# Performance work log

Hardware: AMD Instinct MI355X
Metric: run time of the kernel (lower is better)

## Reference

```python
import jax, jax.numpy as jnp
import numpy as np

B, H, S, D = 8, 8, 2048, 64
NEG = -1e9


def setup_inputs() -> dict:
    key = jax.random.key(0)
    k1, k2, k3, k4 = jax.random.split(key, 4)
    query = jax.random.normal(k1, (B, H, S, D), dtype=jnp.float32)
    kk = jax.random.normal(k2, (B, H, S, D), dtype=jnp.float32)
    value = jax.random.normal(k3, (B, H, S, D), dtype=jnp.float32)
    mask = jax.random.randint(k4, (B, S, S), 0, 2, dtype=jnp.int32)
    return {"query": query, "key": kk, "value": value, "mask": mask}


def reference(query, key, value, mask):
    dk = key.shape[-1]
    # scores: [B,H,S,S] = (q/sqrt(dk)) @ k^T
    scores = jnp.einsum('bhqd,bhkd->bhqk', query / np.sqrt(dk), key)
    # mask broadcast over heads: [B,1,S,S]
    scores = jnp.where(mask[:, None, :, :] == 0, NEG, scores)
    attn = jax.nn.softmax(scores.astype(jnp.float32), axis=-1).astype(query.dtype)
    # dropout is identity in eval/deterministic reference
    return jnp.einsum('bhqk,bhkd->bhqd', attn, value)
```

## Files before the change

kernel.cpp:

```cpp
#include <hip/hip_runtime.h>
#include <hip/hip_bf16.h>
#include <stdint.h>


#define B_ 8
#define H_ 8
#define S_ 2048
#define D_ 64
#define QT 128
#define KT 64
#define NT (S_ / KT)
#define TILE_E (KT * D_)
#define LOG2E 1.44269504088896340736f
#define QSCALE (0.125f * LOG2E)

typedef __bf16 bf16;
typedef bf16 bf16x8 __attribute__((ext_vector_type(8)));
typedef float f32x4 __attribute__((ext_vector_type(4)));
typedef unsigned short ushort8_t __attribute__((ext_vector_type(8)));
typedef unsigned long long u64;

#if __has_builtin(__builtin_amdgcn_exp2f)
#define EXP2(x) __builtin_amdgcn_exp2f(x)
#else
#define EXP2(x) exp2f(x)
#endif

static __device__ __forceinline__ unsigned short bfb(float f) {
    bf16 h = (bf16)f;
    return __builtin_bit_cast(unsigned short, h);
}
static __device__ __forceinline__ int phi_inv(int c) {
    return ((c >> 5) & 1) * 32 + ((c >> 2) & 1) * 16 + ((c >> 4) & 1) * 8 +
           ((c >> 3) & 1) * 4 + (c & 3);
}
static __device__ __forceinline__ void gload16(const unsigned short* g, unsigned short* l) {
    __builtin_amdgcn_global_load_lds(
        (const __attribute__((address_space(1))) unsigned int*)g,
        (__attribute__((address_space(3))) unsigned int*)l, 16, 0, 0);
}

#define KV_BLOCKS (B_ * H_ * NT)

__global__ __launch_bounds__(256) void prep_fused(
    const float* __restrict__ K, const float* __restrict__ V,
    unsigned short* __restrict__ Ko, unsigned short* __restrict__ Vo,
    const int* __restrict__ M, u64* __restrict__ W) {
    const int tid = threadIdx.x;
    if (blockIdx.x >= KV_BLOCKS) {
        const int ln = tid & 63;
        const int w0 = (blockIdx.x - KV_BLOCKS) * 32 + (tid >> 6) * 8;
#pragma unroll
        for (int j = 0; j < 8; ++j) {
            const int v = M[(long)(w0 + j) * 64 + ln];
            const u64 bal = __ballot(v != 0);
            if (ln == 0) W[w0 + j] = bal;
        }
        return;
    }
    if (Ko == nullptr) return;
    __shared__ float Vl[64][65];
    const int t = blockIdx.x & (NT - 1);
    const int bh = blockIdx.x >> 5;
    const float* Kg = K + ((long)bh * S_ + t * 64) * D_;
    const float* Vg = V + ((long)bh * S_ + t * 64) * D_;
    unsigned short* Kout = Ko + ((long)bh * S_ + t * 64) * D_;
    unsigned short* Vout = Vo + (long)bh * D_ * S_ + t * 64;
    {
        const int kv = tid >> 2, d0 = (tid & 3) * 16;
#pragma unroll
        for (int half = 0; half < 2; ++half) {
            const float4 f0 = *(const float4*)(Kg + kv * D_ + d0 + half * 8);
            const float4 f1 = *(const float4*)(Kg + kv * D_ + d0 + half * 8 + 4);
            ushort8_t u;
            u[0] = bfb(f0.x); u[1] = bfb(f0.y); u[2] = bfb(f0.z); u[3] = bfb(f0.w);
            u[4] = bfb(f1.x); u[5] = bfb(f1.y); u[6] = bfb(f1.z); u[7] = bfb(f1.w);
            *(ushort8_t*)(Kout + kv * D_ + d0 + half * 8) = u;
        }
    }
    {
#pragma unroll
        for (int i = 0; i < 4; ++i) {
            const int kv = i * 16 + (tid >> 4);
            const int d4 = (tid & 15) * 4;
            const float4 f = *(const float4*)(Vg + kv * D_ + d4);
            Vl[kv][d4 + 0] = f.x; Vl[kv][d4 + 1] = f.y;
            Vl[kv][d4 + 2] = f.z; Vl[kv][d4 + 3] = f.w;
        }
    }
    __syncthreads();
    {
#pragma unroll
        for (int j = 0; j < 4; ++j) {
            const int chunk = j * 256 + tid;
            const int d = chunk >> 4, q4 = chunk & 15;
            ushort4 w;
            w.x = bfb(Vl[phi_inv(q4 * 4 + 0)][d]);
            w.y = bfb(Vl[phi_inv(q4 * 4 + 1)][d]);
            w.z = bfb(Vl[phi_inv(q4 * 4 + 2)][d]);
            w.w = bfb(Vl[phi_inv(q4 * 4 + 3)][d]);
            *(ushort4*)(Vout + (long)d * S_ + q4 * 4) = w;
        }
    }
}

template <int MODE>
__global__ __launch_bounds__(512, 4) void attn_fwd(
    const float* __restrict__ Q, const float* __restrict__ K,
    const float* __restrict__ V, const int* __restrict__ M,
    const u64* __restrict__ W, const unsigned short* __restrict__ Kp,
    const unsigned short* __restrict__ Vp, float* __restrict__ O)
{
    __shared__ __attribute__((aligned(16))) unsigned short Ks3[4 * TILE_E];
    __shared__ __attribute__((aligned(16))) unsigned short Vt3[4 * TILE_E];

    const int tid = threadIdx.x;
    const int wv = tid >> 6, ln = tid & 63;
    const int col = ln & 15, grp = ln >> 4;

    int bid = blockIdx.x;
    bid = (bid & 7) * 128 + (bid >> 3);
    const int qt = bid & 15;
    const int h = (bid >> 4) & 7;
    const int b = bid >> 7;
    const int qw = qt * QT + wv * 16;

    const float* Qg = Q + ((long)((b * H_ + h) * S_) + qw + col) * D_;
    bf16x8 qf[2];
#pragma unroll
    for (int c = 0; c < 2; ++c) {
        const float4 a0 = *(const float4*)(Qg + c * 32 + grp * 8);
        const float4 a1 = *(const float4*)(Qg + c * 32 + grp * 8 + 4);
        qf[c][0] = (bf16)(a0.x * QSCALE); qf[c][1] = (bf16)(a0.y * QSCALE);
        qf[c][2] = (bf16)(a0.z * QSCALE); qf[c][3] = (bf16)(a0.w * QSCALE);
        qf[c][4] = (bf16)(a1.x * QSCALE); qf[c][5] = (bf16)(a1.y * QSCALE);
        qf[c][6] = (bf16)(a1.z * QSCALE); qf[c][7] = (bf16)(a1.w * QSCALE);
    }
    bf16x8 onesf;
#pragma unroll
    for (int j = 0; j < 8; ++j) onesf[j] = (bf16)1.0f;

    f32x4 oacc[4];
#pragma unroll
    for (int i = 0; i < 4; ++i) oacc[i] = (f32x4){0.f, 0.f, 0.f, 0.f};
    f32x4 accs = (f32x4){0.f, 0.f, 0.f, 0.f};

    const u64* Wg = (MODE >= 1) ? (W + ((long)b * S_ + qw + col) * (S_ / 64)) : nullptr;
    const int* Mg = (MODE == 0) ? (M + ((long)b * S_ + qw + col) * S_) : nullptr;
    const unsigned short* Kbh = Kp + (long)(b * H_ + h) * S_ * D_;
    const unsigned short* Vbh = Vp + (long)(b * H_ + h) * D_ * S_;
    const float* Kf = K + (long)(b * H_ + h) * S_ * D_;
    const float* Vf = V + (long)(b * H_ + h) * S_ * D_;

    const int rl = ln >> 3;
    const int c8 = (ln & 7) ^ rl;
    const int krow = wv * 8 + rl;

    float4 ka[2];
    float va[8];
    const int vd = ln, kg0 = wv;

    auto STAGE_ISSUE = [&](int kv0, int buf) {
        gload16(Kbh + (long)(kv0 + krow) * D_ + c8 * 8, Ks3 + buf * TILE_E + wv * 512);
        gload16(Vbh + (long)krow * S_ + kv0 + c8 * 8, Vt3 + buf * TILE_E + wv * 512);
    };
    auto LOADT = [&](int kv0) {
#pragma unroll
        for (int i = 0; i < 2; ++i) {
            const int idx4 = i * 512 + tid;
            const int row = idx4 >> 4, c4 = idx4 & 15;
            ka[i] = *(const float4*)(Kf + (long)(kv0 + row) * D_ + c4 * 4);
        }
#pragma unroll
        for (int i = 0; i < 2; ++i) {
            const int kg = kg0 + i * 8;
            const int kvn = phi_inv(kg * 4);
#pragma unroll
            for (int j = 0; j < 4; ++j)
                va[i * 4 + j] = Vf[(long)(kv0 + kvn + j) * D_ + vd];
        }
    };
    auto WRITET = [&](int buf) {
#pragma unroll
        for (int i = 0; i < 2; ++i) {
            const int idx4 = i * 512 + tid;
            const int row = idx4 >> 4, c4 = idx4 & 15;
            const int byte = (row * 128 + c4 * 8) ^ ((row & 7) << 4);
            ushort4 w;
            w.x = bfb(ka[i].x); w.y = bfb(ka[i].y);
            w.z = bfb(ka[i].z); w.w = bfb(ka[i].w);
            *(ushort4*)((char*)(Ks3 + buf * TILE_E) + byte) = w;
        }
#pragma unroll
        for (int i = 0; i < 2; ++i) {
            const int kg = kg0 + i * 8;
            const int byte = (vd * 128 + kg * 8) ^ ((vd & 7) << 4);
            ushort4 w;
            w.x = bfb(va[i * 4 + 0]); w.y = bfb(va[i * 4 + 1]);
            w.z = bfb(va[i * 4 + 2]); w.w = bfb(va[i * 4 + 3]);
            *(ushort4*)((char*)(Vt3 + buf * TILE_E) + byte) = w;
        }
    };

    auto QKB = [&](u64 mwfull, const unsigned short* Kc, f32x4* sc) {
        const u64 mws = mwfull >> (grp * 4);
        const unsigned mlo = (unsigned)mws, mhi = (unsigned)(mws >> 32);
#pragma unroll
        for (int blk = 0; blk < 4; ++blk) {
            const unsigned w32 = (blk < 2) ? mlo : mhi;
#pragma unroll
            for (int r = 0; r < 4; ++r) {
                const int bit = (blk & 1) * 16 + r;
                sc[blk][r] = ((w32 >> bit) & 1u) ? 0.0f : -1e9f;
            }
        }
        __builtin_amdgcn_s_setprio(1);
#pragma unroll
        for (int blk = 0; blk < 4; ++blk) {
            const int row = blk * 16 + col;
            const int byte0 = (row * 128 + grp * 16) ^ ((row & 7) << 4);
            const int byte1 = (row * 128 + 64 + grp * 16) ^ ((row & 7) << 4);
            const bf16x8 kf0 = *(const bf16x8*)((const char*)Kc + byte0);
            const bf16x8 kf1 = *(const bf16x8*)((const char*)Kc + byte1);
            sc[blk] = __builtin_amdgcn_mfma_f32_16x16x32_bf16(kf0, qf[0], sc[blk], 0, 0, 0);
            sc[blk] = __builtin_amdgcn_mfma_f32_16x16x32_bf16(kf1, qf[1], sc[blk], 0, 0, 0);
        }
        __builtin_amdgcn_s_setprio(0);
    };
    auto SMPV = [&](f32x4* sc, const unsigned short* Vc) {
        bf16x8 pf[2];
#pragma unroll
        for (int c = 0; c < 2; ++c)
#pragma unroll
            for (int j = 0; j < 8; ++j)
                pf[c][j] = (bf16)EXP2(sc[2 * c + (j >> 2)][j & 3]);
        __builtin_amdgcn_s_setprio(1);
        accs = __builtin_amdgcn_mfma_f32_16x16x32_bf16(pf[0], onesf, accs, 0, 0, 0);
        accs = __builtin_amdgcn_mfma_f32_16x16x32_bf16(pf[1], onesf, accs, 0, 0, 0);
#pragma unroll
        for (int c = 0; c < 2; ++c)
#pragma unroll
            for (int db = 0; db < 4; ++db) {
                const int vrow = db * 16 + col;
                const int byte = (vrow * 128 + c * 64 + grp * 16) ^ ((vrow & 7) << 4);
                const bf16x8 vf = *(const bf16x8*)((const char*)Vc + byte);
                oacc[db] = __builtin_amdgcn_mfma_f32_16x16x32_bf16(pf[c], vf, oacc[db], 0, 0, 0);
            }
        __builtin_amdgcn_s_setprio(0);
    };

#define WAIT2_BAR() do { asm volatile("s_waitcnt vmcnt(2)" ::: "memory"); \
    __builtin_amdgcn_s_barrier(); __builtin_amdgcn_sched_barrier(0); } while (0)
#define WAIT0_BAR() do { asm volatile("s_waitcnt vmcnt(0)" ::: "memory"); \
    __builtin_amdgcn_s_barrier(); __builtin_amdgcn_sched_barrier(0); } while (0)

    if (MODE == 2) {
        f32x4 scA[4], scB[4];
        STAGE_ISSUE(0, 0);
        STAGE_ISSUE(KT, 1);
        WAIT2_BAR();
        {
            const u64 mw0 = Wg[0];
            QKB(mw0, Ks3, scA);
            STAGE_ISSUE(2 * KT, 2);
        }
        WAIT2_BAR();
#pragma unroll 1
        for (int tt = 0; tt < NT - 4; tt += 4) {
#pragma unroll
            for (int j = 0; j < 4; ++j) {
                const int t = tt + j;
                const u64 mwn = Wg[t + 1];
                STAGE_ISSUE((t + 3) * KT, (j + 3) & 3);
                if ((j & 1) == 0) {
                    QKB(mwn, Ks3 + ((j + 1) & 3) * TILE_E, scB);
                    SMPV(scA, Vt3 + j * TILE_E);
                } else {
                    QKB(mwn, Ks3 + ((j + 1) & 3) * TILE_E, scA);
                    SMPV(scB, Vt3 + j * TILE_E);
                }
                WAIT2_BAR();
            }
        }
        {
            const u64 mw29 = Wg[NT - 3];
            STAGE_ISSUE((NT - 1) * KT, (NT - 1) & 3);
            QKB(mw29, Ks3 + ((NT - 3) & 3) * TILE_E, scB);
            SMPV(scA, Vt3 + ((NT - 4) & 3) * TILE_E);
            WAIT2_BAR();
            const u64 mw30 = Wg[NT - 2];
            QKB(mw30, Ks3 + ((NT - 2) & 3) * TILE_E, scA);
            SMPV(scB, Vt3 + ((NT - 3) & 3) * TILE_E);
            WAIT0_BAR();
            const u64 mw31 = Wg[NT - 1];
            QKB(mw31, Ks3 + ((NT - 1) & 3) * TILE_E, scB);
            SMPV(scA, Vt3 + ((NT - 2) & 3) * TILE_E);
            SMPV(scB, Vt3 + ((NT - 1) & 3) * TILE_E);
        }
    } else {
        auto FSTEP = [&](u64 mwfull, int t, const unsigned short* Kc, const unsigned short* Vc) {
            f32x4 sc[4];
            const f32x4 zq = (f32x4){0.f, 0.f, 0.f, 0.f};
#pragma unroll
            for (int blk = 0; blk < 4; ++blk) {
                const int row = blk * 16 + col;
                const int byte0 = (row * 128 + grp * 16) ^ ((row & 7) << 4);
                const int byte1 = (row * 128 + 64 + grp * 16) ^ ((row & 7) << 4);
                const bf16x8 kf0 = *(const bf16x8*)((const char*)Kc + byte0);
                const bf16x8 kf1 = *(const bf16x8*)((const char*)Kc + byte1);
                sc[blk] = __builtin_amdgcn_mfma_f32_16x16x32_bf16(kf0, qf[0], zq, 0, 0, 0);
                sc[blk] = __builtin_amdgcn_mfma_f32_16x16x32_bf16(kf1, qf[1], sc[blk], 0, 0, 0);
            }
            bf16x8 pf[2];
            if (MODE >= 1) {
                const u64 mws = mwfull >> (grp * 4);
                const unsigned mlo = (unsigned)mws, mhi = (unsigned)(mws >> 32);
#pragma unroll
                for (int c = 0; c < 2; ++c)
#pragma unroll
                    for (int j = 0; j < 8; ++j) {
                        const int blk = 2 * c + (j >> 2), r = j & 3;
                        const unsigned w32 = (blk < 2) ? mlo : mhi;
                        const int bit = (blk & 1) * 16 + r;
                        const float s = ((w32 >> bit) & 1u) ? sc[blk][r] : -1e9f;
                        pf[c][j] = (bf16)EXP2(s);
                    }
            } else {
#pragma unroll
                for (int c = 0; c < 2; ++c)
#pragma unroll
                    for (int j = 0; j < 8; ++j) {
                        const int blk = 2 * c + (j >> 2), r = j & 3;
                        const int mv = Mg[t * KT + blk * 16 + grp * 4 + r];
                        const float s = mv ? sc[blk][r] : -1e9f;
                        pf[c][j] = (bf16)EXP2(s);
                    }
            }
            accs = __builtin_amdgcn_mfma_f32_16x16x32_bf16(pf[0], onesf, accs, 0, 0, 0);
            accs = __builtin_amdgcn_mfma_f32_16x16x32_bf16(pf[1], onesf, accs, 0, 0, 0);
#pragma unroll
            for (int c = 0; c < 2; ++c)
#pragma unroll
                for (int db = 0; db < 4; ++db) {
                    const int vrow = db * 16 + col;
                    const int byte = (vrow * 128 + c * 64 + grp * 16) ^ ((vrow & 7) << 4);
                    const bf16x8 vf = *(const bf16x8*)((const char*)Vc + byte);
                    oacc[db] = __builtin_amdgcn_mfma_f32_16x16x32_bf16(pf[c], vf, oacc[db], 0, 0, 0);
                }
        };
        LOADT(0);
        WRITET(0);
        __syncthreads();
#pragma unroll 1
        for (int t = 0; t < NT; t += 2) {
            if (t + 1 < NT) LOADT((t + 1) * KT);
            FSTEP(MODE >= 1 ? Wg[t] : 0ull, t, Ks3, Vt3);
            if (t + 1 < NT) WRITET(1);
            __syncthreads();
            if (t + 2 < NT) LOADT((t + 2) * KT);
            FSTEP(MODE >= 1 ? Wg[t + 1] : 0ull, t + 1, Ks3 + TILE_E, Vt3 + TILE_E);
            if (t + 2 < NT) WRITET(0);
            __syncthreads();
        }
    }

    float* Og = O + ((long)((b * H_ + h) * S_) + qw) * D_;
#pragma unroll
    for (int r = 0; r < 4; ++r) {
        const float inv = 1.0f / accs[r];
#pragma unroll
        for (int db = 0; db < 4; ++db)
            Og[(grp * 4 + r) * D_ + db * 16 + col] = oacc[db][r] * inv;
    }
#undef WAIT2_BAR
#undef WAIT0_BAR
}

extern "C" void kernel_launch(void* const* d_in, const int* in_sizes, int n_in,
                              void* d_out, int out_size, void* d_ws, size_t ws_size,
                              hipStream_t stream) {
    (void)in_sizes; (void)n_in; (void)out_size;
    const float* Q = (const float*)d_in[0];
    const float* K = (const float*)d_in[1];
    const float* V = (const float*)d_in[2];
    const int*   M = (const int*)d_in[3];
    float* O = (float*)d_out;

    const size_t szW = (size_t)B_ * S_ * (S_ / 64) * sizeof(u64);
    const size_t szK = (size_t)B_ * H_ * S_ * D_ * 2;
    const int grid = B_ * H_ * (S_ / QT);
    const int nmaskblk = (B_ * S_ * (S_ / 64)) / 32;

    if (ws_size >= szW + 2 * szK) {
        u64* W = (u64*)d_ws;
        unsigned short* Kp = (unsigned short*)((char*)d_ws + szW);
        unsigned short* Vp = (unsigned short*)((char*)d_ws + szW + szK);
        prep_fused<<<KV_BLOCKS + nmaskblk, 256, 0, stream>>>(K, V, Kp, Vp, M, W);
        attn_fwd<2><<<grid, 512, 0, stream>>>(Q, K, V, M, W, Kp, Vp, O);
    } else if (ws_size >= szW) {
        u64* W = (u64*)d_ws;
        prep_fused<<<KV_BLOCKS + nmaskblk, 256, 0, stream>>>(K, V, nullptr, nullptr, M, W);
        attn_fwd<1><<<grid, 512, 0, stream>>>(Q, K, V, M, W, nullptr, nullptr, O);
    } else {
        attn_fwd<0><<<grid, 512, 0, stream>>>(Q, K, V, M, nullptr, nullptr, nullptr, O);
    }
}
```

Measured before the change: 157.0 us.

## Split main attention path into 256-thread kernel with two query tiles per wave

The workspace path now uses a new attn_main kernel with 4 waves per block, where each wave handles 32 query rows (two 16-row tiles). Each K and V fragment read from LDS feeds MFMAs for both tiles, which halves LDS reads per unit of work. The old software pipeline that overlapped the next tile's QK with the current softmax·V is replaced by a simpler prefetch-2 loop that computes QK and PV in the same step. This raises register pressure and gives up that cross-stage overlap, with the intent of getting more MFMA work per LDS load and per barrier.

```diff
diff --git a/kernel.cpp b/kernel.cpp
--- a/kernel.cpp
+++ b/kernel.cpp
@@ -104,15 +104,203 @@
     }
 }
 
-template <int MODE>
-__global__ __launch_bounds__(512, 4) void attn_fwd(
-    const float* __restrict__ Q, const float* __restrict__ K,
-    const float* __restrict__ V, const int* __restrict__ M,
-    const u64* __restrict__ W, const unsigned short* __restrict__ Kp,
-    const unsigned short* __restrict__ Vp, float* __restrict__ O)
+__global__ __launch_bounds__(256, 2) void attn_main(
+    const float* __restrict__ Q, const u64* __restrict__ W,
+    const unsigned short* __restrict__ Kp, const unsigned short* __restrict__ Vp,
+    float* __restrict__ O)
 {
     __shared__ __attribute__((aligned(16))) unsigned short Ks3[4 * TILE_E];
     __shared__ __attribute__((aligned(16))) unsigned short Vt3[4 * TILE_E];
+
+    const int tid = threadIdx.x;
+    const int wv = tid >> 6, ln = tid & 63;
+    const int col = ln & 15, grp = ln >> 4;
+
+    int bid = blockIdx.x;
+    bid = (bid & 7) * 128 + (bid >> 3);
+    const int qt = bid & 15;
+    const int h = (bid >> 4) & 7;
+    const int b = bid >> 7;
+    const int qa = qt * QT + wv * 32;
+
+    bf16x8 qfa[2], qfb[2];
+    {
+        const float* Qga = Q + ((long)((b * H_ + h) * S_) + qa + col) * D_;
+        const float* Qgb = Qga + 16 * D_;
+#pragma unroll
+        for (int c = 0; c < 2; ++c) {
+            const float4 a0 = *(const float4*)(Qga + c * 32 + grp * 8);
+            const float4 a1 = *(const float4*)(Qga + c * 32 + grp * 8 + 4);
+            qfa[c][0] = (bf16)(a0.x * QSCALE); qfa[c][1] = (bf16)(a0.y * QSCALE);
+            qfa[c][2] = (bf16)(a0.z * QSCALE); qfa[c][3] = (bf16)(a0.w * QSCALE);
+            qfa[c][4] = (bf16)(a1.x * QSCALE); qfa[c][5] = (bf16)(a1.y * QSCALE);
+            qfa[c][6] = (bf16)(a1.z * QSCALE); qfa[c][7] = (bf16)(a1.w * QSCALE);
+            const float4 b0 = *(const float4*)(Qgb + c * 32 + grp * 8);
+            const float4 b1 = *(const float4*)(Qgb + c * 32 + grp * 8 + 4);
+            qfb[c][0] = (bf16)(b0.x * QSCALE); qfb[c][1] = (bf16)(b0.y * QSCALE);
+            qfb[c][2] = (bf16)(b0.z * QSCALE); qfb[c][3] = (bf16)(b0.w * QSCALE);
+            qfb[c][4] = (bf16)(b1.x * QSCALE); qfb[c][5] = (bf16)(b1.y * QSCALE);
+            qfb[c][6] = (bf16)(b1.z * QSCALE); qfb[c][7] = (bf16)(b1.w * QSCALE);
+        }
+    }
+    bf16x8 onesf;
+#pragma unroll
+    for (int j = 0; j < 8; ++j) onesf[j] = (bf16)1.0f;
+
+    f32x4 oaccA[4], oaccB[4];
+#pragma unroll
+    for (int i = 0; i < 4; ++i) {
+        oaccA[i] = (f32x4){0.f, 0.f, 0.f, 0.f};
+        oaccB[i] = (f32x4){0.f, 0.f, 0.f, 0.f};
+    }
+    f32x4 accsA = (f32x4){0.f, 0.f, 0.f, 0.f};
+    f32x4 accsB = (f32x4){0.f, 0.f, 0.f, 0.f};
+
+    const u64* Wa = W + ((long)b * S_ + qa + col) * (S_ / 64);
+    const u64* Wb = Wa + 16 * (S_ / 64);
+    const unsigned short* Kbh = Kp + (long)(b * H_ + h) * S_ * D_;
+    const unsigned short* Vbh = Vp + (long)(b * H_ + h) * D_ * S_;
+
+    const int rl = ln >> 3;
+    const int c8 = (ln & 7) ^ rl;
+
+    auto STAGE_ISSUE = [&](int kv0, int buf) {
+#pragma unroll
+        for (int i = 0; i < 2; ++i) {
+            const int row = i * 32 + wv * 8 + rl;
+            gload16(Kbh + (long)(kv0 + row) * D_ + c8 * 8,
+                    Ks3 + buf * TILE_E + i * 2048 + wv * 512);
+            gload16(Vbh + (long)row * S_ + kv0 + c8 * 8,
+                    Vt3 + buf * TILE_E + i * 2048 + wv * 512);
+        }
+    };
+
+    auto STEP = [&](u64 mwa, u64 mwb, const unsigned short* Kc, const unsigned short* Vc) {
+        f32x4 sa[4], sb[4];
+        {
+            const u64 ma = mwa >> (grp * 4), mb = mwb >> (grp * 4);
+            const unsigned alo = (unsigned)ma, ahi = (unsigned)(ma >> 32);
+            const unsigned blo = (unsigned)mb, bhi = (unsigned)(mb >> 32);
+#pragma unroll
+            for (int blk = 0; blk < 4; ++blk) {
+                const unsigned wa32 = (blk < 2) ? alo : ahi;
+                const unsigned wb32 = (blk < 2) ? blo : bhi;
+#pragma unroll
+                for (int r = 0; r < 4; ++r) {
+                    const int bit = (blk & 1) * 16 + r;
+                    sa[blk][r] = ((wa32 >> bit) & 1u) ? 0.0f : -1e9f;
+                    sb[blk][r] = ((wb32 >> bit) & 1u) ? 0.0f : -1e9f;
+                }
+            }
+        }
+        __builtin_amdgcn_s_setprio(1);
+#pragma unroll
+        for (int blk = 0; blk < 4; ++blk) {
+            const int row = blk * 16 + col;
+            const int byte0 = (row * 128 + grp * 16) ^ ((row & 7) << 4);
+            const int byte1 = (row * 128 + 64 + grp * 16) ^ ((row & 7) << 4);
+            const bf16x8 kf0 = *(const bf16x8*)((const char*)Kc + byte0);
+            const bf16x8 kf1 = *(const bf16x8*)((const char*)Kc + byte1);
+            sa[blk] = __builtin_amdgcn_mfma_f32_16x16x32_bf16(kf0, qfa[0], sa[blk], 0, 0, 0);
+            sa[blk] = __builtin_amdgcn_mfma_f32_16x16x32_bf16(kf1, qfa[1], sa[blk], 0, 0, 0);
+            sb[blk] = __builtin_amdgcn_mfma_f32_16x16x32_bf16(kf0, qfb[0], sb[blk], 0, 0, 0);
+            sb[blk] = __builtin_amdgcn_mfma_f32_16x16x32_bf16(kf1, qfb[1], sb[blk], 0, 0, 0);
+        }
+        __builtin_amdgcn_s_setprio(0);
+        bf16x8 pa[2], pb[2];
+#pragma unroll
+        for (int c = 0; c < 2; ++c)
+#pragma unroll
+            for (int j = 0; j < 8; ++j) {
+                const int blk = 2 * c + (j >> 2), r = j & 3;
+                pa[c][j] = (bf16)EXP2(sa[blk][r]);
+                pb[c][j] = (bf16)EXP2(sb[blk][r]);
+            }
+        __builtin_amdgcn_s_setprio(1);
+        accsA = __builtin_amdgcn_mfma_f32_16x16x32_bf16(pa[0], onesf, accsA, 0, 0, 0);
+        accsA = __builtin_amdgcn_mfma_f32_16x16x32_bf16(pa[1], onesf, accsA, 0, 0, 0);
+        accsB = __builtin_amdgcn_mfma_f32_16x16x32_bf16(pb[0], onesf, accsB, 0, 0, 0);
+        accsB = __builtin_amdgcn_mfma_f32_16x16x32_bf16(pb[1], onesf, accsB, 0, 0, 0);
+#pragma unroll
+        for (int c = 0; c < 2; ++c)
+#pragma unroll
+            for (int db = 0; db < 4; ++db) {
+                const int vrow = db * 16 + col;
+                const int byte = (vrow * 128 + c * 64 + grp * 16) ^ ((vrow & 7) << 4);
+                const bf16x8 vf = *(const bf16x8*)((const char*)Vc + byte);
+                oaccA[db] = __builtin_amdgcn_mfma_f32_16x16x32_bf16(pa[c], vf, oaccA[db], 0, 0, 0);
+                oaccB[db] = __builtin_amdgcn_mfma_f32_16x16x32_bf16(pb[c], vf, oaccB[db], 0, 0, 0);
+            }
+        __builtin_amdgcn_s_setprio(0);
+    };
+
+#define WAIT4_BAR() do { asm volatile("s_waitcnt vmcnt(4)" ::: "memory"); \
+    __builtin_amdgcn_s_barrier(); __builtin_amdgcn_sched_barrier(0); } while (0)
+#define WAIT0_BAR() do { asm volatile("s_waitcnt vmcnt(0)" ::: "memory"); \
+    __builtin_amdgcn_s_barrier(); __builtin_amdgcn_sched_barrier(0); } while (0)
+
+    STAGE_ISSUE(0, 0);
+    STAGE_ISSUE(KT, 1);
+    WAIT4_BAR();
+
+#pragma unroll 1
+    for (int tt = 0; tt < NT - 4; tt += 4) {
+#pragma unroll
+        for (int j = 0; j < 4; ++j) {
+            const int t = tt + j;
+            const u64 mwa = Wa[t], mwb = Wb[t];
+            STAGE_ISSUE((t + 2) * KT, (j + 2) & 3);
+            STEP(mwa, mwb, Ks3 + j * TILE_E, Vt3 + j * TILE_E);
+            WAIT4_BAR();
+        }
+    }
+    {
+        {
+            const u64 mwa = Wa[NT - 4], mwb = Wb[NT - 4];
+            STAGE_ISSUE((NT - 2) * KT, (NT - 2) & 3);
+            STEP(mwa, mwb, Ks3 + ((NT - 4) & 3) * TILE_E, Vt3 + ((NT - 4) & 3) * TILE_E);
+            WAIT4_BAR();
+        }
+        {
+            const u64 mwa = Wa[NT - 3], mwb = Wb[NT - 3];
+            STAGE_ISSUE((NT - 1) * KT, (NT - 1) & 3);
+            STEP(mwa, mwb, Ks3 + ((NT - 3) & 3) * TILE_E, Vt3 + ((NT - 3) & 3) * TILE_E);
+            WAIT4_BAR();
+        }
+        {
+            const u64 mwa = Wa[NT - 2], mwb = Wb[NT - 2];
+            STEP(mwa, mwb, Ks3 + ((NT - 2) & 3) * TILE_E, Vt3 + ((NT - 2) & 3) * TILE_E);
+            WAIT0_BAR();
+        }
+        {
+            const u64 mwa = Wa[NT - 1], mwb = Wb[NT - 1];
+            STEP(mwa, mwb, Ks3 + ((NT - 1) & 3) * TILE_E, Vt3 + ((NT - 1) & 3) * TILE_E);
+        }
+    }
+
+    float* Oa = O + ((long)((b * H_ + h) * S_) + qa) * D_;
+#pragma unroll
+    for (int r = 0; r < 4; ++r) {
+        const float ia = 1.0f / accsA[r];
+        const float ib = 1.0f / accsB[r];
+#pragma unroll
+        for (int db = 0; db < 4; ++db) {
+            Oa[(grp * 4 + r) * D_ + db * 16 + col] = oaccA[db][r] * ia;
+            Oa[(16 + grp * 4 + r) * D_ + db * 16 + col] = oaccB[db][r] * ib;
+        }
+    }
+#undef WAIT4_BAR
+#undef WAIT0_BAR
+}
+
+template <int MODE>
+__global__ __launch_bounds__(512, 4) void attn_fb(
+    const float* __restrict__ Q, const float* __restrict__ K,
+    const float* __restrict__ V, const int* __restrict__ M,
+    const u64* __restrict__ W, float* __restrict__ O)
+{
+    __shared__ __attribute__((aligned(16))) unsigned short Ks2[2 * TILE_E];
+    __shared__ __attribute__((aligned(16))) unsigned short Vt2[2 * TILE_E];
 
     const int tid = threadIdx.x;
     const int wv = tid >> 6, ln = tid & 63;
@@ -147,23 +335,13 @@
 
     const u64* Wg = (MODE >= 1) ? (W + ((long)b * S_ + qw + col) * (S_ / 64)) : nullptr;
     const int* Mg = (MODE == 0) ? (M + ((long)b * S_ + qw + col) * S_) : nullptr;
-    const unsigned short* Kbh = Kp + (long)(b * H_ + h) * S_ * D_;
-    const unsigned short* Vbh = Vp + (long)(b * H_ + h) * D_ * S_;
     const float* Kf = K + (long)(b * H_ + h) * S_ * D_;
     const float* Vf = V + (long)(b * H_ + h) * S_ * D_;
-
-    const int rl = ln >> 3;
-    const int c8 = (ln & 7) ^ rl;
-    const int krow = wv * 8 + rl;
 
     float4 ka[2];
     float va[8];
     const int vd = ln, kg0 = wv;
 
-    auto STAGE_ISSUE = [&](int kv0, int buf) {
-        gload16(Kbh + (long)(kv0 + krow) * D_ + c8 * 8, Ks3 + buf * TILE_E + wv * 512);
-        gload16(Vbh + (long)krow * S_ + kv0 + c8 * 8, Vt3 + buf * TILE_E + wv * 512);
-    };
     auto LOADT = [&](int kv0) {
 #pragma unroll
         for (int i = 0; i < 2; ++i) {
@@ -189,7 +367,7 @@
             ushort4 w;
             w.x = bfb(ka[i].x); w.y = bfb(ka[i].y);
             w.z = bfb(ka[i].z); w.w = bfb(ka[i].w);
-            *(ushort4*)((char*)(Ks3 + buf * TILE_E) + byte) = w;
+            *(ushort4*)((char*)(Ks2 + buf * TILE_E) + byte) = w;
         }
 #pragma unroll
         for (int i = 0; i < 2; ++i) {
@@ -198,23 +376,12 @@
             ushort4 w;
             w.x = bfb(va[i * 4 + 0]); w.y = bfb(va[i * 4 + 1]);
             w.z = bfb(va[i * 4 + 2]); w.w = bfb(va[i * 4 + 3]);
-            *(ushort4*)((char*)(Vt3 + buf * TILE_E) + byte) = w;
+            *(ushort4*)((char*)(Vt2 + buf * TILE_E) + byte) = w;
         }
     };
-
-    auto QKB = [&](u64 mwfull, const unsigned short* Kc, f32x4* sc) {
-        const u64 mws = mwfull >> (grp * 4);
-        const unsigned mlo = (unsigned)mws, mhi = (unsigned)(mws >> 32);
-#pragma unroll
-        for (int blk = 0; blk < 4; ++blk) {
-            const unsigned w32 = (blk < 2) ? mlo : mhi;
-#pragma unroll
-            for (int r = 0; r < 4; ++r) {
-                const int bit = (blk & 1) * 16 + r;
-                sc[blk][r] = ((w32 >> bit) & 1u) ? 0.0f : -1e9f;
-            }
-        }
-        __builtin_amdgcn_s_setprio(1);
+    auto FSTEP = [&](u64 mwfull, int t, const unsigned short* Kc, const unsigned short* Vc) {
+        f32x4 sc[4];
+        const f32x4 zq = (f32x4){0.f, 0.f, 0.f, 0.f};
 #pragma unroll
         for (int blk = 0; blk < 4; ++blk) {
             const int row = blk * 16 + col;
@@ -222,19 +389,34 @@
             const int byte1 = (row * 128 + 64 + grp * 16) ^ ((row & 7) << 4);
             const bf16x8 kf0 = *(const bf16x8*)((const char*)Kc + byte0);
             const bf16x8 kf1 = *(const bf16x8*)((const char*)Kc + byte1);
-            sc[blk] = __builtin_amdgcn_mfma_f32_16x16x32_bf16(kf0, qf[0], sc[blk], 0, 0, 0);
+            sc[blk] = __builtin_amdgcn_mfma_f32_16x16x32_bf16(kf0, qf[0], zq, 0, 0, 0);
             sc[blk] = __builtin_amdgcn_mfma_f32_16x16x32_bf16(kf1, qf[1], sc[blk], 0, 0, 0);
         }
-        __builtin_amdgcn_s_setprio(0);
-    };
-    auto SMPV = [&](f32x4* sc, const unsigned short* Vc) {
         bf16x8 pf[2];
-#pragma unroll
-        for (int c = 0; c < 2; ++c)
-#pragma unroll
-            for (int j = 0; j < 8; ++j)
-                pf[c][j] = (bf16)EXP2(sc[2 * c + (j >> 2)][j & 3]);
-        __builtin_amdgcn_s_setprio(1);
+        if (MODE >= 1) {
+            const u64 mws = mwfull >> (grp * 4);
+            const unsigned mlo = (unsigned)mws, mhi = (unsigned)(mws >> 32);
+#pragma unroll
+            for (int c = 0; c < 2; ++c)
+#pragma unroll
+                for (int j = 0; j < 8; ++j) {
+                    const int blk = 2 * c + (j >> 2), r = j & 3;
+                    const unsigned w32 = (blk < 2) ? mlo : mhi;
+                    const int bit = (blk & 1) * 16 + r;
+                    const float s = ((w32 >> bit) & 1u) ? sc[blk][r] : -1e9f;
+                    pf[c][j] = (bf16)EXP2(s);
+                }
+        } else {
+#pragma unroll
+            for (int c = 0; c < 2; ++c)
+#pragma unroll
+                for (int j = 0; j < 8; ++j) {
+                    const int blk = 2 * c + (j >> 2), r = j & 3;
+                    const int mv = Mg[t * KT + blk * 16 + grp * 4 + r];
+                    const float s = mv ? sc[blk][r] : -1e9f;
+                    pf[c][j] = (bf16)EXP2(s);
+                }
+        }
         accs = __builtin_amdgcn_mfma_f32_16x16x32_bf16(pf[0], onesf, accs, 0, 0, 0);
         accs = __builtin_amdgcn_mfma_f32_16x16x32_bf16(pf[1], onesf, accs, 0, 0, 0);
 #pragma unroll
@@ -246,122 +428,21 @@
                 const bf16x8 vf = *(const bf16x8*)((const char*)Vc + byte);
                 oacc[db] = __builtin_amdgcn_mfma_f32_16x16x32_bf16(pf[c], vf, oacc[db], 0, 0, 0);
             }
-        __builtin_amdgcn_s_setprio(0);
     };
 
-#define WAIT2_BAR() do { asm volatile("s_waitcnt vmcnt(2)" ::: "memory"); \
-    __builtin_amdgcn_s_barrier(); __builtin_amdgcn_sched_barrier(0); } while (0)
-#define WAIT0_BAR() do { asm volatile("s_waitcnt vmcnt(0)" ::: "memory"); \
-    __builtin_amdgcn_s_barrier(); __builtin_amdgcn_sched_barrier(0); } while (0)
-
-    if (MODE == 2) {
-        f32x4 scA[4], scB[4];
-        STAGE_ISSUE(0, 0);
-        STAGE_ISSUE(KT, 1);
-        WAIT2_BAR();
-        {
-            const u64 mw0 = Wg[0];
-            QKB(mw0, Ks3, scA);
-            STAGE_ISSUE(2 * KT, 2);
-        }
-        WAIT2_BAR();
+    LOADT(0);
+    WRITET(0);
+    __syncthreads();
 #pragma unroll 1
-        for (int tt = 0; tt < NT - 4; tt += 4) {
-#pragma unroll
-            for (int j = 0; j < 4; ++j) {
-                const int t = tt + j;
-                const u64 mwn = Wg[t + 1];
-                STAGE_ISSUE((t + 3) * KT, (j + 3) & 3);
-                if ((j & 1) == 0) {
-                    QKB(mwn, Ks3 + ((j + 1) & 3) * TILE_E, scB);
-                    SMPV(scA, Vt3 + j * TILE_E);
-                } else {
-                    QKB(mwn, Ks3 + ((j + 1) & 3) * TILE_E, scA);
-                    SMPV(scB, Vt3 + j * TILE_E);
-                }
-                WAIT2_BAR();
-            }
-        }
-        {
-            const u64 mw29 = Wg[NT - 3];
-            STAGE_ISSUE((NT - 1) * KT, (NT - 1) & 3);
-            QKB(mw29, Ks3 + ((NT - 3) & 3) * TILE_E, scB);
-            SMPV(scA, Vt3 + ((NT - 4) & 3) * TILE_E);
-            WAIT2_BAR();
-            const u64 mw30 = Wg[NT - 2];
-            QKB(mw30, Ks3 + ((NT - 2) & 3) * TILE_E, scA);
-            SMPV(scB, Vt3 + ((NT - 3) & 3) * TILE_E);
-            WAIT0_BAR();
-            const u64 mw31 = Wg[NT - 1];
-            QKB(mw31, Ks3 + ((NT - 1) & 3) * TILE_E, scB);
-            SMPV(scA, Vt3 + ((NT - 2) & 3) * TILE_E);
-            SMPV(scB, Vt3 + ((NT - 1) & 3) * TILE_E);
-        }
-    } else {
-        auto FSTEP = [&](u64 mwfull, int t, const unsigned short* Kc, const unsigned short* Vc) {
-            f32x4 sc[4];
-            const f32x4 zq = (f32x4){0.f, 0.f, 0.f, 0.f};
-#pragma unroll
-            for (int blk = 0; blk < 4; ++blk) {
-                const int row = blk * 16 + col;
-                const int byte0 = (row * 128 + grp * 16) ^ ((row & 7) << 4);
-                const int byte1 = (row * 128 + 64 + grp * 16) ^ ((row & 7) << 4);
-                const bf16x8 kf0 = *(const bf16x8*)((const char*)Kc + byte0);
-                const bf16x8 kf1 = *(const bf16x8*)((const char*)Kc + byte1);
-                sc[blk] = __builtin_amdgcn_mfma_f32_16x16x32_bf16(kf0, qf[0], zq, 0, 0, 0);
-                sc[blk] = __builtin_amdgcn_mfma_f32_16x16x32_bf16(kf1, qf[1], sc[blk], 0, 0, 0);
-            }
-            bf16x8 pf[2];
-            if (MODE >= 1) {
-                const u64 mws = mwfull >> (grp * 4);
-                const unsigned mlo = (unsigned)mws, mhi = (unsigned)(mws >> 32);
-#pragma unroll
-                for (int c = 0; c < 2; ++c)
-#pragma unroll
-                    for (int j = 0; j < 8; ++j) {
-                        const int blk = 2 * c + (j >> 2), r = j & 3;
-                        const unsigned w32 = (blk < 2) ? mlo : mhi;
-                        const int bit = (blk & 1) * 16 + r;
-                        const float s = ((w32 >> bit) & 1u) ? sc[blk][r] : -1e9f;
-                        pf[c][j] = (bf16)EXP2(s);
-                    }
-            } else {
-#pragma unroll
-                for (int c = 0; c < 2; ++c)
-#pragma unroll
-                    for (int j = 0; j < 8; ++j) {
-                        const int blk = 2 * c + (j >> 2), r = j & 3;
-                        const int mv = Mg[t * KT + blk * 16 + grp * 4 + r];
-                        const float s = mv ? sc[blk][r] : -1e9f;
-                        pf[c][j] = (bf16)EXP2(s);
-                    }
-            }
-            accs = __builtin_amdgcn_mfma_f32_16x16x32_bf16(pf[0], onesf, accs, 0, 0, 0);
-            accs = __builtin_amdgcn_mfma_f32_16x16x32_bf16(pf[1], onesf, accs, 0, 0, 0);
-#pragma unroll
-            for (int c = 0; c < 2; ++c)
-#pragma unroll
-                for (int db = 0; db < 4; ++db) {
-                    const int vrow = db * 16 + col;
-                    const int byte = (vrow * 128 + c * 64 + grp * 16) ^ ((vrow & 7) << 4);
-                    const bf16x8 vf = *(const bf16x8*)((const char*)Vc + byte);
-                    oacc[db] = __builtin_amdgcn_mfma_f32_16x16x32_bf16(pf[c], vf, oacc[db], 0, 0, 0);
-                }
-        };
-        LOADT(0);
-        WRITET(0);
+    for (int t = 0; t < NT; t += 2) {
+        if (t + 1 < NT) LOADT((t + 1) * KT);
+        FSTEP(MODE >= 1 ? Wg[t] : 0ull, t, Ks2, Vt2);
+        if (t + 1 < NT) WRITET(1);
         __syncthreads();
-#pragma unroll 1
-        for (int t = 0; t < NT; t += 2) {
-            if (t + 1 < NT) LOADT((t + 1) * KT);
-            FSTEP(MODE >= 1 ? Wg[t] : 0ull, t, Ks3, Vt3);
-            if (t + 1 < NT) WRITET(1);
-            __syncthreads();
-            if (t + 2 < NT) LOADT((t + 2) * KT);
-            FSTEP(MODE >= 1 ? Wg[t + 1] : 0ull, t + 1, Ks3 + TILE_E, Vt3 + TILE_E);
-            if (t + 2 < NT) WRITET(0);
-            __syncthreads();
-        }
+        if (t + 2 < NT) LOADT((t + 2) * KT);
+        FSTEP(MODE >= 1 ? Wg[t + 1] : 0ull, t + 1, Ks2 + TILE_E, Vt2 + TILE_E);
+        if (t + 2 < NT) WRITET(0);
+        __syncthreads();
     }
 
     float* Og = O + ((long)((b * H_ + h) * S_) + qw) * D_;
@@ -372,8 +453,6 @@
         for (int db = 0; db < 4; ++db)
             Og[(grp * 4 + r) * D_ + db * 16 + col] = oacc[db][r] * inv;
     }
-#undef WAIT2_BAR
-#undef WAIT0_BAR
 }
 
 extern "C" void kernel_launch(void* const* d_in, const int* in_sizes, int n_in,
@@ -396,12 +475,12 @@
         unsigned short* Kp = (unsigned short*)((char*)d_ws + szW);
         unsigned short* Vp = (unsigned short*)((char*)d_ws + szW + szK);
         prep_fused<<<KV_BLOCKS + nmaskblk, 256, 0, stream>>>(K, V, Kp, Vp, M, W);
-        attn_fwd<2><<<grid, 512, 0, stream>>>(Q, K, V, M, W, Kp, Vp, O);
+        attn_main<<<grid, 256, 0, stream>>>(Q, W, Kp, Vp, O);
     } else if (ws_size >= szW) {
         u64* W = (u64*)d_ws;
         prep_fused<<<KV_BLOCKS + nmaskblk, 256, 0, stream>>>(K, V, nullptr, nullptr, M, W);
-        attn_fwd<1><<<grid, 512, 0, stream>>>(Q, K, V, M, W, nullptr, nullptr, O);
+        attn_fb<1><<<grid, 512, 0, stream>>>(Q, K, V, M, W, O);
     } else {
-        attn_fwd<0><<<grid, 512, 0, stream>>>(Q, K, V, M, nullptr, nullptr, nullptr, O);
-    }
-}
+        attn_fb<0><<<grid, 512, 0, stream>>>(Q, K, V, M, nullptr, O);
+    }
+}
```

Result: slower. 164.8 us (+5.0%).

## Replace 4-stage software-pipelined attention loop with simple double buffer at higher occupancy

Applied to the files above, without the earlier changes.

The main path drops the 4-buffer, 2-ahead pipeline in which QK of the next tile overlapped softmax/PV of the current one. It now uses a plain 2-buffer loop with one async stage in flight and a full vmcnt(0) barrier each step. LDS is halved and launch bounds go from 4 to 8 blocks per SM, so occupancy is meant to hide latency instead of explicit pipelining. The risk is exposed load latency and more barrier stalls per tile. The fallback modes are split into a separate kernel and are otherwise unchanged.

```diff
diff --git a/kernel.cpp b/kernel.cpp
--- a/kernel.cpp
+++ b/kernel.cpp
@@ -104,15 +104,13 @@
     }
 }
 
-template <int MODE>
-__global__ __launch_bounds__(512, 4) void attn_fwd(
-    const float* __restrict__ Q, const float* __restrict__ K,
-    const float* __restrict__ V, const int* __restrict__ M,
-    const u64* __restrict__ W, const unsigned short* __restrict__ Kp,
-    const unsigned short* __restrict__ Vp, float* __restrict__ O)
+__global__ __launch_bounds__(512, 8) void attn_main(
+    const float* __restrict__ Q, const u64* __restrict__ W,
+    const unsigned short* __restrict__ Kp, const unsigned short* __restrict__ Vp,
+    float* __restrict__ O)
 {
-    __shared__ __attribute__((aligned(16))) unsigned short Ks3[4 * TILE_E];
-    __shared__ __attribute__((aligned(16))) unsigned short Vt3[4 * TILE_E];
+    __shared__ __attribute__((aligned(16))) unsigned short Ks2[2 * TILE_E];
+    __shared__ __attribute__((aligned(16))) unsigned short Vt2[2 * TILE_E];
 
     const int tid = threadIdx.x;
     const int wv = tid >> 6, ln = tid & 63;
@@ -145,73 +143,32 @@
     for (int i = 0; i < 4; ++i) oacc[i] = (f32x4){0.f, 0.f, 0.f, 0.f};
     f32x4 accs = (f32x4){0.f, 0.f, 0.f, 0.f};
 
-    const u64* Wg = (MODE >= 1) ? (W + ((long)b * S_ + qw + col) * (S_ / 64)) : nullptr;
-    const int* Mg = (MODE == 0) ? (M + ((long)b * S_ + qw + col) * S_) : nullptr;
+    const u64* Wg = W + ((long)b * S_ + qw + col) * (S_ / 64);
     const unsigned short* Kbh = Kp + (long)(b * H_ + h) * S_ * D_;
     const unsigned short* Vbh = Vp + (long)(b * H_ + h) * D_ * S_;
-    const float* Kf = K + (long)(b * H_ + h) * S_ * D_;
-    const float* Vf = V + (long)(b * H_ + h) * S_ * D_;
-
-    const int rl = ln >> 3;
-    const int c8 = (ln & 7) ^ rl;
-    const int krow = wv * 8 + rl;
-
-    float4 ka[2];
-    float va[8];
-    const int vd = ln, kg0 = wv;
+
+    const int srow = tid >> 3;
+    const int rl = srow & 7;
+    const int c8 = (tid & 7) ^ rl;
 
     auto STAGE_ISSUE = [&](int kv0, int buf) {
-        gload16(Kbh + (long)(kv0 + krow) * D_ + c8 * 8, Ks3 + buf * TILE_E + wv * 512);
-        gload16(Vbh + (long)krow * S_ + kv0 + c8 * 8, Vt3 + buf * TILE_E + wv * 512);
+        gload16(Kbh + (long)(kv0 + srow) * D_ + c8 * 8, Ks2 + buf * TILE_E + tid * 8);
+        gload16(Vbh + (long)srow * S_ + kv0 + c8 * 8, Vt2 + buf * TILE_E + tid * 8);
     };
-    auto LOADT = [&](int kv0) {
-#pragma unroll
-        for (int i = 0; i < 2; ++i) {
-            const int idx4 = i * 512 + tid;
-            const int row = idx4 >> 4, c4 = idx4 & 15;
-            ka[i] = *(const float4*)(Kf + (long)(kv0 + row) * D_ + c4 * 4);
-        }
-#pragma unroll
-        for (int i = 0; i < 2; ++i) {
-            const int kg = kg0 + i * 8;
-            const int kvn = phi_inv(kg * 4);
-#pragma unroll
-            for (int j = 0; j < 4; ++j)
-                va[i * 4 + j] = Vf[(long)(kv0 + kvn + j) * D_ + vd];
-        }
-    };
-    auto WRITET = [&](int buf) {
-#pragma unroll
-        for (int i = 0; i < 2; ++i) {
-            const int idx4 = i * 512 + tid;
-            const int row = idx4 >> 4, c4 = idx4 & 15;
-            const int byte = (row * 128 + c4 * 8) ^ ((row & 7) << 4);
-            ushort4 w;
-            w.x = bfb(ka[i].x); w.y = bfb(ka[i].y);
-            w.z = bfb(ka[i].z); w.w = bfb(ka[i].w);
-            *(ushort4*)((char*)(Ks3 + buf * TILE_E) + byte) = w;
-        }
-#pragma unroll
-        for (int i = 0; i < 2; ++i) {
-            const int kg = kg0 + i * 8;
-            const int byte = (vd * 128 + kg * 8) ^ ((vd & 7) << 4);
-            ushort4 w;
-            w.x = bfb(va[i * 4 + 0]); w.y = bfb(va[i * 4 + 1]);
-            w.z = bfb(va[i * 4 + 2]); w.w = bfb(va[i * 4 + 3]);
-            *(ushort4*)((char*)(Vt3 + buf * TILE_E) + byte) = w;
-        }
-    };
-
-    auto QKB = [&](u64 mwfull, const unsigned short* Kc, f32x4* sc) {
-        const u64 mws = mwfull >> (grp * 4);
-        const unsigned mlo = (unsigned)mws, mhi = (unsigned)(mws >> 32);
-#pragma unroll
-        for (int blk = 0; blk < 4; ++blk) {
-            const unsigned w32 = (blk < 2) ? mlo : mhi;
-#pragma unroll
-            for (int r = 0; r < 4; ++r) {
-                const int bit = (blk & 1) * 16 + r;
-                sc[blk][r] = ((w32 >> bit) & 1u) ? 0.0f : -1e9f;
+
+    auto STEP = [&](u64 mwfull, const unsigned short* Kc, const unsigned short* Vc) {
+        f32x4 sc[4];
+        {
+            const u64 mws = mwfull >> (grp * 4);
+            const unsigned mlo = (unsigned)mws, mhi = (unsigned)(mws >> 32);
+#pragma unroll
+            for (int blk = 0; blk < 4; ++blk) {
+                const unsigned w32 = (blk < 2) ? mlo : mhi;
+#pragma unroll
+                for (int r = 0; r < 4; ++r) {
+                    const int bit = (blk & 1) * 16 + r;
+                    sc[blk][r] = ((w32 >> bit) & 1u) ? 0.0f : -1e9f;
+                }
             }
         }
         __builtin_amdgcn_s_setprio(1);
@@ -226,8 +183,6 @@
             sc[blk] = __builtin_amdgcn_mfma_f32_16x16x32_bf16(kf1, qf[1], sc[blk], 0, 0, 0);
         }
         __builtin_amdgcn_s_setprio(0);
-    };
-    auto SMPV = [&](f32x4* sc, const unsigned short* Vc) {
         bf16x8 pf[2];
 #pragma unroll
         for (int c = 0; c < 2; ++c)
@@ -249,118 +204,25 @@
         __builtin_amdgcn_s_setprio(0);
     };
 
-#define WAIT2_BAR() do { asm volatile("s_waitcnt vmcnt(2)" ::: "memory"); \
-    __builtin_amdgcn_s_barrier(); __builtin_amdgcn_sched_barrier(0); } while (0)
 #define WAIT0_BAR() do { asm volatile("s_waitcnt vmcnt(0)" ::: "memory"); \
     __builtin_amdgcn_s_barrier(); __builtin_amdgcn_sched_barrier(0); } while (0)
 
-    if (MODE == 2) {
-        f32x4 scA[4], scB[4];
-        STAGE_ISSUE(0, 0);
-        STAGE_ISSUE(KT, 1);
-        WAIT2_BAR();
+    STAGE_ISSUE(0, 0);
+    WAIT0_BAR();
+
+#pragma unroll 1
+    for (int t = 0; t < NT; t += 2) {
         {
-            const u64 mw0 = Wg[0];
-            QKB(mw0, Ks3, scA);
-            STAGE_ISSUE(2 * KT, 2);
-        }
-        WAIT2_BAR();
-#pragma unroll 1
-        for (int tt = 0; tt < NT - 4; tt += 4) {
-#pragma unroll
-            for (int j = 0; j < 4; ++j) {
-                const int t = tt + j;
-                const u64 mwn = Wg[t + 1];
-                STAGE_ISSUE((t + 3) * KT, (j + 3) & 3);
-                if ((j & 1) == 0) {
-                    QKB(mwn, Ks3 + ((j + 1) & 3) * TILE_E, scB);
-                    SMPV(scA, Vt3 + j * TILE_E);
-                } else {
-                    QKB(mwn, Ks3 + ((j + 1) & 3) * TILE_E, scA);
-                    SMPV(scB, Vt3 + j * TILE_E);
-                }
-                WAIT2_BAR();
-            }
+            const u64 mw = Wg[t];
+            if (t + 1 < NT) STAGE_ISSUE((t + 1) * KT, 1);
+            STEP(mw, Ks2, Vt2);
+            WAIT0_BAR();
         }
         {
-            const u64 mw29 = Wg[NT - 3];
-            STAGE_ISSUE((NT - 1) * KT, (NT - 1) & 3);
-            QKB(mw29, Ks3 + ((NT - 3) & 3) * TILE_E, scB);
-            SMPV(scA, Vt3 + ((NT - 4) & 3) * TILE_E);
-            WAIT2_BAR();
-            const u64 mw30 = Wg[NT - 2];
-            QKB(mw30, Ks3 + ((NT - 2) & 3) * TILE_E, scA);
-            SMPV(scB, Vt3 + ((NT - 3) & 3) * TILE_E);
+            const u64 mw = Wg[t + 1];
+            if (t + 2 < NT) STAGE_ISSUE((t + 2) * KT, 0);
+            STEP(mw, Ks2 + TILE_E, Vt2 + TILE_E);
             WAIT0_BAR();
-            const u64 mw31 = Wg[NT - 1];
-            QKB(mw31, Ks3 + ((NT - 1) & 3) * TILE_E, scB);
-            SMPV(scA, Vt3 + ((NT - 2) & 3) * TILE_E);
-            SMPV(scB, Vt3 + ((NT - 1) & 3) * TILE_E);
-        }
-    } else {
-        auto FSTEP = [&](u64 mwfull, int t, const unsigned short* Kc, const unsigned short* Vc) {
-            f32x4 sc[4];
-            const f32x4 zq = (f32x4){0.f, 0.f, 0.f, 0.f};
-#pragma unroll
-            for (int blk = 0; blk < 4; ++blk) {
-                const int row = blk * 16 + col;
-                const int byte0 = (row * 128 + grp * 16) ^ ((row & 7) << 4);
-                const int byte1 = (row * 128 + 64 + grp * 16) ^ ((row & 7) << 4);
-                const bf16x8 kf0 = *(const bf16x8*)((const char*)Kc + byte0);
-                const bf16x8 kf1 = *(const bf16x8*)((const char*)Kc + byte1);
-                sc[blk] = __builtin_amdgcn_mfma_f32_16x16x32_bf16(kf0, qf[0], zq, 0, 0, 0);
-                sc[blk] = __builtin_amdgcn_mfma_f32_16x16x32_bf16(kf1, qf[1], sc[blk], 0, 0, 0);
-            }
-            bf16x8 pf[2];
-            if (MODE >= 1) {
-                const u64 mws = mwfull >> (grp * 4);
-                const unsigned mlo = (unsigned)mws, mhi = (unsigned)(mws >> 32);
-#pragma unroll
-                for (int c = 0; c < 2; ++c)
-#pragma unroll
-                    for (int j = 0; j < 8; ++j) {
-                        const int blk = 2 * c + (j >> 2), r = j & 3;
-                        const unsigned w32 = (blk < 2) ? mlo : mhi;
-                        const int bit = (blk & 1) * 16 + r;
-                        const float s = ((w32 >> bit) & 1u) ? sc[blk][r] : -1e9f;
-                        pf[c][j] = (bf16)EXP2(s);
-                    }
-            } else {
-#pragma unroll
-                for (int c = 0; c < 2; ++c)
-#pragma unroll
-                    for (int j = 0; j < 8; ++j) {
-                        const int blk = 2 * c + (j >> 2), r = j & 3;
-                        const int mv = Mg[t * KT + blk * 16 + grp * 4 + r];
-                        const float s = mv ? sc[blk][r] : -1e9f;
-                        pf[c][j] = (bf16)EXP2(s);
-                    }
-            }
-            accs = __builtin_amdgcn_mfma_f32_16x16x32_bf16(pf[0], onesf, accs, 0, 0, 0);
-            accs = __builtin_amdgcn_mfma_f32_16x16x32_bf16(pf[1], onesf, accs, 0, 0, 0);
-#pragma unroll
-            for (int c = 0; c < 2; ++c)
-#pragma unroll
-                for (int db = 0; db < 4; ++db) {
-                    const int vrow = db * 16 + col;
-                    const int byte = (vrow * 128 + c * 64 + grp * 16) ^ ((vrow & 7) << 4);
-                    const bf16x8 vf = *(const bf16x8*)((const char*)Vc + byte);
-                    oacc[db] = __builtin_amdgcn_mfma_f32_16x16x32_bf16(pf[c], vf, oacc[db], 0, 0, 0);
-                }
-        };
-        LOADT(0);
-        WRITET(0);
-        __syncthreads();
-#pragma unroll 1
-        for (int t = 0; t < NT; t += 2) {
-            if (t + 1 < NT) LOADT((t + 1) * KT);
-            FSTEP(MODE >= 1 ? Wg[t] : 0ull, t, Ks3, Vt3);
-            if (t + 1 < NT) WRITET(1);
-            __syncthreads();
-            if (t + 2 < NT) LOADT((t + 2) * KT);
-            FSTEP(MODE >= 1 ? Wg[t + 1] : 0ull, t + 1, Ks3 + TILE_E, Vt3 + TILE_E);
-            if (t + 2 < NT) WRITET(0);
-            __syncthreads();
         }
     }
 
@@ -372,8 +234,169 @@
         for (int db = 0; db < 4; ++db)
             Og[(grp * 4 + r) * D_ + db * 16 + col] = oacc[db][r] * inv;
     }
-#undef WAIT2_BAR
 #undef WAIT0_BAR
+}
+
+template <int MODE>
+__global__ __launch_bounds__(512, 4) void attn_fb(
+    const float* __restrict__ Q, const float* __restrict__ K,
+    const float* __restrict__ V, const int* __restrict__ M,
+    const u64* __restrict__ W, float* __restrict__ O)
+{
+    __shared__ __attribute__((aligned(16))) unsigned short Ks2[2 * TILE_E];
+    __shared__ __attribute__((aligned(16))) unsigned short Vt2[2 * TILE_E];
+
+    const int tid = threadIdx.x;
+    const int wv = tid >> 6, ln = tid & 63;
+    const int col = ln & 15, grp = ln >> 4;
+
+    int bid = blockIdx.x;
+    bid = (bid & 7) * 128 + (bid >> 3);
+    const int qt = bid & 15;
+    const int h = (bid >> 4) & 7;
+    const int b = bid >> 7;
+    const int qw = qt * 128 + wv * 16;
+
+    const float* Qg = Q + ((long)((b * H_ + h) * S_) + qw + col) * D_;
+    bf16x8 qf[2];
+#pragma unroll
+    for (int c = 0; c < 2; ++c) {
+        const float4 a0 = *(const float4*)(Qg + c * 32 + grp * 8);
+        const float4 a1 = *(const float4*)(Qg + c * 32 + grp * 8 + 4);
+        qf[c][0] = (bf16)(a0.x * QSCALE); qf[c][1] = (bf16)(a0.y * QSCALE);
+        qf[c][2] = (bf16)(a0.z * QSCALE); qf[c][3] = (bf16)(a0.w * QSCALE);
+        qf[c][4] = (bf16)(a1.x * QSCALE); qf[c][5] = (bf16)(a1.y * QSCALE);
+        qf[c][6] = (bf16)(a1.z * QSCALE); qf[c][7] = (bf16)(a1.w * QSCALE);
+    }
+    bf16x8 onesf;
+#pragma unroll
+    for (int j = 0; j < 8; ++j) onesf[j] = (bf16)1.0f;
+
+    f32x4 oacc[4];
+#pragma unroll
+    for (int i = 0; i < 4; ++i) oacc[i] = (f32x4){0.f, 0.f, 0.f, 0.f};
+    f32x4 accs = (f32x4){0.f, 0.f, 0.f, 0.f};
+
+    const u64* Wg = (MODE >= 1) ? (W + ((long)b * S_ + qw + col) * (S_ / 64)) : nullptr;
+    const int* Mg = (MODE == 0) ? (M + ((long)b * S_ + qw + col) * S_) : nullptr;
+    const float* Kf = K + (long)(b * H_ + h) * S_ * D_;
+    const float* Vf = V + (long)(b * H_ + h) * S_ * D_;
+
+    float4 ka[2];
+    float va[8];
+    const int vd = ln, kg0 = wv;
+
+    auto LOADT = [&](int kv0) {
+#pragma unroll
+        for (int i = 0; i < 2; ++i) {
+            const int idx4 = i * 512 + tid;
+            const int row = idx4 >> 4, c4 = idx4 & 15;
+            ka[i] = *(const float4*)(Kf + (long)(kv0 + row) * D_ + c4 * 4);
+        }
+#pragma unroll
+        for (int i = 0; i < 2; ++i) {
+            const int kg = kg0 + i * 8;
+            const int kvn = phi_inv(kg * 4);
+#pragma unroll
+            for (int j = 0; j < 4; ++j)
+                va[i * 4 + j] = Vf[(long)(kv0 + kvn + j) * D_ + vd];
+        }
+    };
+    auto WRITET = [&](int buf) {
+#pragma unroll
+        for (int i = 0; i < 2; ++i) {
+            const int idx4 = i * 512 + tid;
+            const int row = idx4 >> 4, c4 = idx4 & 15;
+            const int byte = (row * 128 + c4 * 8) ^ ((row & 7) << 4);
+            ushort4 w;
+            w.x = bfb(ka[i].x); w.y = bfb(ka[i].y);
+            w.z = bfb(ka[i].z); w.w = bfb(ka[i].w);
+            *(ushort4*)((char*)(Ks2 + buf * TILE_E) + byte) = w;
+        }
+#pragma unroll
+        for (int i = 0; i < 2; ++i) {
+            const int kg = kg0 + i * 8;
+            const int byte = (vd * 128 + kg * 8) ^ ((vd & 7) << 4);
+            ushort4 w;
+            w.x = bfb(va[i * 4 + 0]); w.y = bfb(va[i * 4 + 1]);
+            w.z = bfb(va[i * 4 + 2]); w.w = bfb(va[i * 4 + 3]);
+            *(ushort4*)((char*)(Vt2 + buf * TILE_E) + byte) = w;
+        }
+    };
+    auto FSTEP = [&](u64 mwfull, int t, const unsigned short* Kc, const unsigned short* Vc) {
+        f32x4 sc[4];
+        const f32x4 zq = (f32x4){0.f, 0.f, 0.f, 0.f};
+#pragma unroll
+        for (int blk = 0; blk < 4; ++blk) {
+            const int row = blk * 16 + col;
+            const int byte0 = (row * 128 + grp * 16) ^ ((row & 7) << 4);
+            const int byte1 = (row * 128 + 64 + grp * 16) ^ ((row & 7) << 4);
+            const bf16x8 kf0 = *(const bf16x8*)((const char*)Kc + byte0);
+            const bf16x8 kf1 = *(const bf16x8*)((const char*)Kc + byte1);
+            sc[blk] = __builtin_amdgcn_mfma_f32_16x16x32_bf16(kf0, qf[0], zq, 0, 0, 0);
+            sc[blk] = __builtin_amdgcn_mfma_f32_16x16x32_bf16(kf1, qf[1], sc[blk], 0, 0, 0);
+        }
+        bf16x8 pf[2];
+        if (MODE >= 1) {
+            const u64 mws = mwfull >> (grp * 4);
+            const unsigned mlo = (unsigned)mws, mhi = (unsigned)(mws >> 32);
+#pragma unroll
+            for (int c = 0; c < 2; ++c)
+#pragma unroll
+                for (int j = 0; j < 8; ++j) {
+                    const int blk = 2 * c + (j >> 2), r = j & 3;
+                    const unsigned w32 = (blk < 2) ? mlo : mhi;
+                    const int bit = (blk & 1) * 16 + r;
+                    const float s = ((w32 >> bit) & 1u) ? sc[blk][r] : -1e9f;
+                    pf[c][j] = (bf16)EXP2(s);
+                }
+        } else {
+#pragma unroll
+            for (int c = 0; c < 2; ++c)
+#pragma unroll
+                for (int j = 0; j < 8; ++j) {
+                    const int blk = 2 * c + (j >> 2), r = j & 3;
+                    const int mv = Mg[t * KT + blk * 16 + grp * 4 + r];
+                    const float s = mv ? sc[blk][r] : -1e9f;
+                    pf[c][j] = (bf16)EXP2(s);
+                }
+        }
+        accs = __builtin_amdgcn_mfma_f32_16x16x32_bf16(pf[0], onesf, accs, 0, 0, 0);
+        accs = __builtin_amdgcn_mfma_f32_16x16x32_bf16(pf[1], onesf, accs, 0, 0, 0);
+#pragma unroll
+        for (int c = 0; c < 2; ++c)
+#pragma unroll
+            for (int db = 0; db < 4; ++db) {
+                const int vrow = db * 16 + col;
+                const int byte = (vrow * 128 + c * 64 + grp * 16) ^ ((vrow & 7) << 4);
+                const bf16x8 vf = *(const bf16x8*)((const char*)Vc + byte);
+                oacc[db] = __builtin_amdgcn_mfma_f32_16x16x32_bf16(pf[c], vf, oacc[db], 0, 0, 0);
+            }
+    };
+
+    LOADT(0);
+    WRITET(0);
+    __syncthreads();
+#pragma unroll 1
+    for (int t = 0; t < NT; t += 2) {
+        if (t + 1 < NT) LOADT((t + 1) * KT);
+        FSTEP(MODE >= 1 ? Wg[t] : 0ull, t, Ks2, Vt2);
+        if (t + 1 < NT) WRITET(1);
+        __syncthreads();
+        if (t + 2 < NT) LOADT((t + 2) * KT);
+        FSTEP(MODE >= 1 ? Wg[t + 1] : 0ull, t + 1, Ks2 + TILE_E, Vt2 + TILE_E);
+        if (t + 2 < NT) WRITET(0);
+        __syncthreads();
+    }
+
+    float* Og = O + ((long)((b * H_ + h) * S_) + qw) * D_;
+#pragma unroll
+    for (int r = 0; r < 4; ++r) {
+        const float inv = 1.0f / accs[r];
+#pragma unroll
+        for (int db = 0; db < 4; ++db)
+            Og[(grp * 4 + r) * D_ + db * 16 + col] = oacc[db][r] * inv;
+    }
 }
 
 extern "C" void kernel_launch(void* const* d_in, const int* in_sizes, int n_in,
@@ -388,7 +411,6 @@
 
     const size_t szW = (size_t)B_ * S_ * (S_ / 64) * sizeof(u64);
     const size_t szK = (size_t)B_ * H_ * S_ * D_ * 2;
-    const int grid = B_ * H_ * (S_ / QT);
     const int nmaskblk = (B_ * S_ * (S_ / 64)) / 32;
 
     if (ws_size >= szW + 2 * szK) {
@@ -396,12 +418,12 @@
         unsigned short* Kp = (unsigned short*)((char*)d_ws + szW);
         unsigned short* Vp = (unsigned short*)((char*)d_ws + szW + szK);
         prep_fused<<<KV_BLOCKS + nmaskblk, 256, 0, stream>>>(K, V, Kp, Vp, M, W);
-        attn_fwd<2><<<grid, 512, 0, stream>>>(Q, K, V, M, W, Kp, Vp, O);
+        attn_main<<<B_ * H_ * (S_ / QT), 512, 0, stream>>>(Q, W, Kp, Vp, O);
     } else if (ws_size >= szW) {
         u64* W = (u64*)d_ws;
         prep_fused<<<KV_BLOCKS + nmaskblk, 256, 0, stream>>>(K, V, nullptr, nullptr, M, W);
-        attn_fwd<1><<<grid, 512, 0, stream>>>(Q, K, V, M, W, nullptr, nullptr, O);
+        attn_fb<1><<<1024, 512, 0, stream>>>(Q, K, V, M, W, O);
     } else {
-        attn_fwd<0><<<grid, 512, 0, stream>>>(Q, K, V, M, nullptr, nullptr, nullptr, O);
-    }
-}
+        attn_fb<0><<<1024, 512, 0, stream>>>(Q, K, V, M, nullptr, O);
+    }
+}
```

New measurement: 302.5 us. 1.93x slower.
